# Kernel optimization log

Hardware: AMD Instinct MI355X
Metric: run time of the kernel (lower is better)

## Reference

```python
import jax, jax.numpy as jnp
import numpy as np
from functools import partial

N_TRAIN, N_FEAT, N_HID, ENC = 4096, 64, 256, 256
GH, AH, N_ANTES, MAX_LEN = 256, 64, 32768, 32


def setup_inputs() -> dict:
    key = jax.random.key(0)
    ks = jax.random.split(key, 14)
    sc = 0.05
    r = lambda k, shp: (jax.random.normal(k, shp, jnp.float32) * sc)
    return {
        'context': jax.random.normal(ks[0], (N_TRAIN, N_FEAT), jnp.float32),
        'S': jax.random.uniform(ks[1], (N_TRAIN, N_ANTES), jnp.float32),
        'enc_W1': r(ks[2], (N_FEAT, N_HID)), 'enc_b1': r(ks[3], (N_HID,)),
        'enc_W2': r(ks[4], (N_HID, ENC)), 'enc_b2': r(ks[5], (ENC,)),
        'W_ih': r(ks[6], (4 * GH, ENC)), 'W_hh': r(ks[7], (4 * GH, GH)),
        'b_ih': r(ks[8], (4 * GH,)), 'b_hh': r(ks[9], (4 * GH,)),
        'att_W1': r(ks[10], (N_TRAIN + GH, AH)), 'att_b1': r(ks[11], (AH,)),
        'att_w2': r(ks[12], (AH,)), 'att_b2': r(ks[13], (1,)),
        'max_len': MAX_LEN,
    }


def reference(context, S, enc_W1, enc_b1, enc_W2, enc_b2,
              W_ih, W_hh, b_ih, b_hh, att_W1, att_b1, att_w2, att_b2,
              max_len):
    n_train = context.shape[0]
    gh = W_hh.shape[1]
    # context encoder: Linear -> ReLU -> Linear  => phi [n_train, enc_dim]
    phi = jax.nn.relu(context @ enc_W1 + enc_b1) @ enc_W2 + enc_b2
    # LSTM input is phi at every step -> precompute input projection once
    x_proj = phi @ W_ih.T + b_ih + b_hh              # [n_train, 4*gh]
    # attention Linear over cat([S^T, e_t]) == S^T @ W1_S + e_t @ W1_h
    # S^T @ W1_S is step-invariant: precompute once  [n_antes, ah]
    S_proj = S.T @ att_W1[:n_train]
    W1_h = att_W1[n_train:]                          # [gh, ah]

    def step(carry, _):
        h, c = carry                                 # [n_train, gh] each
        gates = x_proj + h @ W_hh.T                  # [n_train, 4*gh]
        i, f, g, o = jnp.split(gates, 4, axis=-1)    # PyTorch gate order ifgo
        i, f, o = jax.nn.sigmoid(i), jax.nn.sigmoid(f), jax.nn.sigmoid(o)
        c = f * c + i * jnp.tanh(g)
        h = o * jnp.tanh(c)
        e_t = h.mean(axis=0)                         # mean over batch, [gh]
        hid = jax.nn.relu(S_proj + e_t @ W1_h + att_b1)   # [n_antes, ah]
        scores = hid @ att_w2 + att_b2[0]            # [n_antes]
        return (h, c), scores

    h0 = jnp.zeros((n_train, gh), x_proj.dtype)
    c0 = jnp.zeros((n_train, gh), x_proj.dtype)
    _, scores = jax.lax.scan(step, (h0, c0), None, length=max_len)
    idx = jnp.argmax(scores, axis=-1)                # d[t] = A[idx[t]]
    return scores, idx
```

## Files before the change

kernel.cpp:

```cpp
#include <hip/hip_runtime.h>
#include <hip/hip_bf16.h>
#include <math.h>

#define N_TRAIN 4096
#define N_FEAT  64
#define NHID    256
#define ENC     256
#define GH      256
#define AH      64
#define NANTES  32768
#define TSTEPS  32

#define SSTR 528

typedef __attribute__((ext_vector_type(8))) short bf16x8;
typedef __attribute__((ext_vector_type(4))) float f32x4;

#define BMFMA(a_, b_, c_) __builtin_amdgcn_mfma_f32_16x16x32_bf16(a_, b_, c_, 0, 0, 0)

__device__ __forceinline__ float sigmoidf_(float x) {
    return 1.0f / (1.0f + __expf(-x));
}
__device__ __forceinline__ float tanhf_(float x) {
    return 1.0f - 2.0f / (__expf(2.0f * x) + 1.0f);
}
__device__ __forceinline__ unsigned short f2bf_rne(float x) {
    unsigned int u = __float_as_uint(x);
    unsigned int r = u + 0x7FFFu + ((u >> 16) & 1u);
    return (unsigned short)(r >> 16);
}
__device__ __forceinline__ float bf2f(unsigned short b) {
    return __uint_as_float(((unsigned int)b) << 16);
}

__device__ __forceinline__ void async16(const void* g, void* l) {
    __builtin_amdgcn_global_load_lds(
        (const __attribute__((address_space(1))) void*)g,
        (__attribute__((address_space(3))) void*)l, 16, 0, 0);
}

__global__ void zero_kernel(float* __restrict__ esum) {
    int tid = blockIdx.x * blockDim.x + threadIdx.x;
    for (int i = tid; i < TSTEPS * GH; i += gridDim.x * blockDim.x)
        esum[i] = 0.0f;
}

__global__ void pack_whh(const float* __restrict__ Whh,
                         unsigned short* __restrict__ hi)
{
    int g = blockIdx.x * 256 + threadIdx.x;
    if (g >= 64 * 8 * 64) return;
    int lane  = g & 63;
    int ks    = (g >> 6) & 7;
    int ntile = g >> 9;
    int n  = ntile * 16 + (lane & 15);
    int k0 = ks * 32 + (lane >> 4) * 8;
    const float* src = Whh + n * 256 + k0;
    #pragma unroll
    for (int j = 0; j < 8; ++j)
        hi[g * 8 + j] = f2bf_rne(src[j]);
}

__global__ void pack_wa(const float* __restrict__ attW1,
                        unsigned short* __restrict__ hi,
                        unsigned short* __restrict__ lo)
{
    int g = blockIdx.x * 256 + threadIdx.x;
    if (g >= 4 * 128 * 64) return;
    int lane = g & 63;
    int ks   = (g >> 6) & 127;
    int ct   = g >> 13;
    int n  = ct * 16 + (lane & 15);
    int k0 = ks * 32 + (lane >> 4) * 8;
    const float* src = attW1 + (size_t)k0 * AH + n;
    #pragma unroll
    for (int j = 0; j < 8; ++j) {
        float x = src[(size_t)j * AH];
        unsigned short h16 = f2bf_rne(x);
        hi[g * 8 + j] = h16;
        lo[g * 8 + j] = f2bf_rne(x - bf2f(h16));
    }
}

__global__ __launch_bounds__(512, 2) void lstm_kernel(
    const float* __restrict__ ctx,
    const float* __restrict__ encW1, const float* __restrict__ encb1,
    const float* __restrict__ encW2, const float* __restrict__ encb2,
    const float* __restrict__ Wih,
    const float* __restrict__ bih,  const float* __restrict__ bhh,
    const unsigned short* __restrict__ Wph,
    float* __restrict__ esum)
{
    __shared__ char pool[98304];
    __shared__ short hhi[2][16 * 256];
    __shared__ short hlo[2][16 * 256];

    float* sbuf = (float*)pool;

    const int tid   = threadIdx.x;
    const int j     = tid & 255;
    const int rh    = tid >> 8;
    const int rbase = rh * 8;
    const int r0    = blockIdx.x * 16;

    {
        float acc[8];
        float b = encb1[j];
        #pragma unroll
        for (int r = 0; r < 8; ++r) acc[r] = b;
        for (int k = 0; k < N_FEAT; ++k) {
            float w = encW1[k * NHID + j];
            #pragma unroll
            for (int r = 0; r < 8; ++r)
                acc[r] = fmaf(ctx[(r0 + rbase + r) * N_FEAT + k], w, acc[r]);
        }
        #pragma unroll
        for (int r = 0; r < 8; ++r)
            sbuf[(rbase + r) * SSTR + j] = fmaxf(acc[r], 0.0f);
    }
    __syncthreads();

    {
        float p[8];
        float b = encb2[j];
        #pragma unroll
        for (int r = 0; r < 8; ++r) p[r] = b;
        for (int k = 0; k < NHID; ++k) {
            float w = encW2[k * ENC + j];
            #pragma unroll
            for (int r = 0; r < 8; ++r)
                p[r] = fmaf(sbuf[(rbase + r) * SSTR + k], w, p[r]);
        }
        __syncthreads();
        #pragma unroll
        for (int r = 0; r < 8; ++r)
            sbuf[(rbase + r) * SSTR + 264 + j] = p[r];
    }
    __syncthreads();

    float xp[4][8];
    #pragma unroll
    for (int g = 0; g < 4; ++g) {
        int m = g * 256 + j;
        float b = bih[m] + bhh[m];
        #pragma unroll
        for (int r = 0; r < 8; ++r) xp[g][r] = b;
        const float4* wrow = (const float4*)(Wih + m * ENC);
        for (int k4 = 0; k4 < ENC / 4; ++k4) {
            float4 wv = wrow[k4];
            #pragma unroll
            for (int r = 0; r < 8; ++r) {
                const float* ph = &sbuf[(rbase + r) * SSTR + 264 + k4 * 4];
                float v = xp[g][r];
                v = fmaf(ph[0], wv.x, v);
                v = fmaf(ph[1], wv.y, v);
                v = fmaf(ph[2], wv.z, v);
                v = fmaf(ph[3], wv.w, v);
                xp[g][r] = v;
            }
        }
    }
    __syncthreads();

    const int w    = tid >> 6;
    const int l    = tid & 63;
    const int col  = l & 15;
    const int kp   = l >> 4;
    const int arow = col;
    const int asw  = (arow & 7) << 3;

    f32x4 xpf[4][2];
    #pragma unroll 1
    for (int g = 0; g < 4; ++g) {
        #pragma unroll
        for (int r = 0; r < 8; ++r)
            sbuf[(rbase + r) * SSTR + j] = xp[g][r];
        __syncthreads();
        #pragma unroll
        for (int u = 0; u < 2; ++u)
            #pragma unroll
            for (int q = 0; q < 4; ++q)
                xpf[g][u][q] = sbuf[(kp * 4 + q) * SSTR + w * 32 + u * 16 + col];
        __syncthreads();
    }

    for (int i = tid; i < 16 * 256; i += 512) { hhi[0][i] = 0; hlo[0][i] = 0; }
    __syncthreads();

    const unsigned short* Bh = Wph + (size_t)l * 8;
    char* ra = pool + (w * 3 + 0) * 4096;
    char* rb = pool + (w * 3 + 1) * 4096;
    char* rc = pool + (w * 3 + 2) * 4096;
    const size_t lane16 = (size_t)l * 16;

#define ISSUE(base, gj) do {                                                 \
        const int u_ = (gj) >> 3, ks2_ = (gj) & 7;                           \
        _Pragma("unroll") for (int g_ = 0; g_ < 4; ++g_) {                   \
            const unsigned short* gp_ = Bh +                                 \
                (size_t)(((16 * g_ + 2 * w + u_) * 8 + ks2_) * 64) * 8;      \
            async16(gp_, (base) + g_ * 1024);                                \
        }                                                                    \
    } while (0)

#define CNS(base, gi) do {                                                   \
        asm volatile("s_waitcnt vmcnt(8)" ::: "memory");                     \
        __builtin_amdgcn_sched_barrier(0);                                   \
        const char* p_ = (base) + lane16;                                    \
        bf16x8 f0 = *(const bf16x8*)(p_);                                    \
        bf16x8 f1 = *(const bf16x8*)(p_ + 1024);                             \
        bf16x8 f2 = *(const bf16x8*)(p_ + 2048);                             \
        bf16x8 f3 = *(const bf16x8*)(p_ + 3072);                             \
        const int ks_ = (gi) & 7;                                            \
        bf16x8 ah = *(const bf16x8*)&Ahi[arow * 256 +                        \
                        ((ks_ * 32 + kp * 8) ^ asw)];                        \
        bf16x8 al = *(const bf16x8*)&Alo[arow * 256 +                        \
                        ((ks_ * 32 + kp * 8) ^ asw)];                        \
        acc[0] = BMFMA(al, f0, acc[0]); acc[0] = BMFMA(ah, f0, acc[0]);      \
        acc[1] = BMFMA(al, f1, acc[1]); acc[1] = BMFMA(ah, f1, acc[1]);      \
        acc[2] = BMFMA(al, f2, acc[2]); acc[2] = BMFMA(ah, f2, acc[2]);      \
        acc[3] = BMFMA(al, f3, acc[3]); acc[3] = BMFMA(ah, f3, acc[3]);      \
        asm volatile("" ::: "memory");                                       \
        ISSUE(base, ((gi) + 3) & 15);                                        \
    } while (0)

#define POINTW(u_) do {                                                      \
        float s = 0.0f;                                                      \
        _Pragma("unroll") for (int q = 0; q < 4; ++q) {                      \
            float iv = sigmoidf_(acc[0][q]);                                 \
            float fv = sigmoidf_(acc[1][q]);                                 \
            float gv = tanhf_   (acc[2][q]);                                 \
            float ov = sigmoidf_(acc[3][q]);                                 \
            c[u_][q] = fv * c[u_][q] + iv * gv;                              \
            float hv = ov * tanhf_(c[u_][q]);                                \
            s += hv;                                                         \
            unsigned short h16 = f2bf_rne(hv);                               \
            float lof = hv - bf2f(h16);                                      \
            int row  = kp * 4 + q;                                           \
            int hcol = w * 32 + (u_) * 16 + col;                             \
            int sidx = row * 256 + (hcol ^ ((row & 7) << 3));                \
            Nhi[sidx] = (short)h16;                                          \
            Nlo[sidx] = (short)f2bf_rne(lof);                                \
        }                                                                    \
        su[u_] = s;                                                          \
    } while (0)

    ISSUE(ra, 0); ISSUE(rb, 1); ISSUE(rc, 2);

    float c[2][4];
    #pragma unroll
    for (int u = 0; u < 2; ++u)
        #pragma unroll
        for (int q = 0; q < 4; ++q) c[u][q] = 0.0f;

    for (int t = 0; t < TSTEPS; ++t) {
        const short* Ahi = hhi[t & 1];
        const short* Alo = hlo[t & 1];
        short* Nhi = hhi[(t + 1) & 1];
        short* Nlo = hlo[(t + 1) & 1];

        float su[2];
        f32x4 acc[4];

        #pragma unroll
        for (int g = 0; g < 4; ++g) acc[g] = xpf[g][0];
        CNS(ra, 0); CNS(rb, 1); CNS(rc, 2); CNS(ra, 3);
        CNS(rb, 4); CNS(rc, 5); CNS(ra, 6); CNS(rb, 7);
        POINTW(0);

        #pragma unroll
        for (int g = 0; g < 4; ++g) acc[g] = xpf[g][1];
        CNS(rc, 8);  CNS(ra, 9);  CNS(rb, 10); CNS(rc, 11);
        CNS(ra, 12); CNS(rb, 13); CNS(rc, 14); CNS(ra, 15);
        POINTW(1);

        #pragma unroll
        for (int u = 0; u < 2; ++u) {
            float v = su[u];
            v += __shfl_xor(v, 16);
            v += __shfl_xor(v, 32);
            if (l < 16)
                atomicAdd(&esum[t * GH + w * 32 + u * 16 + l], v);
        }

        asm volatile("s_waitcnt lgkmcnt(0)" ::: "memory");
        __builtin_amdgcn_s_barrier();
        __builtin_amdgcn_sched_barrier(0);
        asm volatile("" ::: "memory");

        char* tp = ra; ra = rb; rb = rc; rc = tp;
    }
#undef ISSUE
#undef CNS
#undef POINTW
}

__global__ void proj_kernel(const float* __restrict__ esum,
                            const float* __restrict__ attW1,
                            const float* __restrict__ attb1,
                            float* __restrict__ proj)
{
    __shared__ float part[4][AH];
    const int t   = blockIdx.x;
    const int cix = threadIdx.x & 63;
    const int g   = threadIdx.x >> 6;
    float a = 0.0f;
    #pragma unroll 4
    for (int k = g * 64; k < g * 64 + 64; ++k) {
        float e = esum[t * GH + k] * (1.0f / (float)N_TRAIN);
        a = fmaf(e, attW1[(size_t)(N_TRAIN + k) * AH + cix], a);
    }
    part[g][cix] = a;
    __syncthreads();
    if (threadIdx.x < AH)
        proj[t * AH + cix] = part[0][cix] + part[1][cix] + part[2][cix] +
                             part[3][cix] + attb1[cix];
}

__global__ __launch_bounds__(512, 4) void scores_kernel(
    const float* __restrict__ S,
    const unsigned short* __restrict__ Wah,
    const unsigned short* __restrict__ Wal,
    const float* __restrict__ proj,
    const float* __restrict__ attw2,
    const float* __restrict__ attb2,
    float* __restrict__ out)
{
    __shared__ float projl[TSTEPS * AH];
    __shared__ float w2l[AH];

    const int tid   = threadIdx.x;
    const int wv    = tid >> 6;
    const int l     = tid & 63;
    const int kp    = l >> 4;
    const int atile = blockIdx.x * 128 + wv * 16;
    const int an    = atile + (l & 15);

    f32x4 acc[4];
    #pragma unroll
    for (int ct = 0; ct < 4; ++ct) acc[ct] = (f32x4){0.f, 0.f, 0.f, 0.f};

    const float* Sp = S + an;
    const unsigned short* Bh = Wah + (size_t)l * 8;
    const unsigned short* Bl = Wal + (size_t)l * 8;

#define LOADS(dst, ks_) do {                                                 \
        _Pragma("unroll") for (int jj = 0; jj < 8; ++jj)                     \
            dst[jj] = Sp[(size_t)(32 * (ks_) + kp * 8 + jj) * NANTES];       \
    } while (0)

    float sA[8], sB[8];
    LOADS(sA, 0);
    LOADS(sB, 1);

    #pragma unroll 2
    for (int ks = 0; ks < 128; ++ks) {
        bf16x8 bh[4], bl[4];
        #pragma unroll
        for (int ct = 0; ct < 4; ++ct) {
            size_t off = (size_t)((ct * 128 + ks) * 64) * 8;
            bh[ct] = *(const bf16x8*)(Bh + off);
            bl[ct] = *(const bf16x8*)(Bl + off);
        }

        float* cur = (ks & 1) ? sB : sA;
        bf16x8 ah, al;
        #pragma unroll
        for (int jj = 0; jj < 8; ++jj) {
            float x = cur[jj];
            unsigned short h16 = f2bf_rne(x);
            ah[jj] = (short)h16;
            al[jj] = (short)f2bf_rne(x - bf2f(h16));
        }

        if (ks < 126) LOADS(cur, ks + 2);

        #pragma unroll
        for (int ct = 0; ct < 4; ++ct) {
            acc[ct] = BMFMA(al, bl[ct], acc[ct]);
            acc[ct] = BMFMA(al, bh[ct], acc[ct]);
            acc[ct] = BMFMA(ah, bl[ct], acc[ct]);
            acc[ct] = BMFMA(ah, bh[ct], acc[ct]);
        }
    }
#undef LOADS

    for (int i = tid; i < TSTEPS * AH; i += 512) projl[i] = proj[i];
    if (tid < AH) w2l[tid] = attw2[tid];
    __syncthreads();

    const float b2v = attb2[0];
    const int cn = l & 15;
    #pragma unroll 1
    for (int t = 0; t < TSTEPS; ++t) {
        #pragma unroll
        for (int q = 0; q < 4; ++q) {
            float sc = 0.0f;
            #pragma unroll
            for (int ct = 0; ct < 4; ++ct) {
                int colg = ct * 16 + cn;
                sc += fmaxf(acc[ct][q] + projl[t * AH + colg], 0.0f) * w2l[colg];
            }
            sc += __shfl_xor(sc, 1);
            sc += __shfl_xor(sc, 2);
            sc += __shfl_xor(sc, 4);
            sc += __shfl_xor(sc, 8);
            if (cn == 0)
                out[(size_t)t * NANTES + atile + kp * 4 + q] = sc + b2v;
        }
    }
}

__global__ void argmax_kernel(const float* __restrict__ scores,
                              float* __restrict__ out)
{
    __shared__ float bv[256];
    __shared__ int   bidx[256];
    const int t = blockIdx.x, tid = threadIdx.x;
    float best = -INFINITY;
    int   bi   = 0x7fffffff;
    for (int a = tid; a < NANTES; a += 256) {
        float v = scores[(size_t)t * NANTES + a];
        if (v > best) { best = v; bi = a; }
    }
    bv[tid] = best; bidx[tid] = bi;
    __syncthreads();
    for (int s = 128; s > 0; s >>= 1) {
        if (tid < s) {
            if (bv[tid + s] > bv[tid] ||
                (bv[tid + s] == bv[tid] && bidx[tid + s] < bidx[tid])) {
                bv[tid] = bv[tid + s];
                bidx[tid] = bidx[tid + s];
            }
        }
        __syncthreads();
    }
    if (tid == 0)
        out[(size_t)TSTEPS * NANTES + t] = (float)bidx[0];
}

extern "C" void kernel_launch(void* const* d_in, const int* in_sizes, int n_in,
                              void* d_out, int out_size, void* d_ws, size_t ws_size,
                              hipStream_t stream)
{
    const float* ctx   = (const float*)d_in[0];
    const float* S     = (const float*)d_in[1];
    const float* encW1 = (const float*)d_in[2];
    const float* encb1 = (const float*)d_in[3];
    const float* encW2 = (const float*)d_in[4];
    const float* encb2 = (const float*)d_in[5];
    const float* Wih   = (const float*)d_in[6];
    const float* Whh   = (const float*)d_in[7];
    const float* bih   = (const float*)d_in[8];
    const float* bhh   = (const float*)d_in[9];
    const float* attW1 = (const float*)d_in[10];
    const float* attb1 = (const float*)d_in[11];
    const float* attw2 = (const float*)d_in[12];
    const float* attb2 = (const float*)d_in[13];

    char* ws = (char*)d_ws;
    float* esum = (float*)ws;
    float* proj = (float*)(ws + 32768);
    unsigned short* Wph = (unsigned short*)(ws + 40960);
    unsigned short* Wah = (unsigned short*)(ws + 40960 + 524288);
    unsigned short* Wal = (unsigned short*)(ws + 40960 + 1048576);
    float* out  = (float*)d_out;

    zero_kernel<<<dim3(8), dim3(256), 0, stream>>>(esum);
    pack_whh<<<dim3(128), dim3(256), 0, stream>>>(Whh, Wph);
    pack_wa<<<dim3(128), dim3(256), 0, stream>>>(attW1, Wah, Wal);
    lstm_kernel<<<dim3(N_TRAIN / 16), dim3(512), 0, stream>>>(
        ctx, encW1, encb1, encW2, encb2, Wih, bih, bhh, Wph, esum);
    proj_kernel<<<dim3(TSTEPS), dim3(256), 0, stream>>>(esum, attW1, attb1, proj);
    scores_kernel<<<dim3(NANTES / 128), dim3(512), 0, stream>>>(
        S, Wah, Wal, proj, attw2, attb2, out);
    argmax_kernel<<<dim3(TSTEPS), dim3(256), 0, stream>>>(out, out);
}
```

Before: 583.8 us.

## Double-buffer two k-slices per stage in LSTM recurrence and drop lo*lo MFMA term

The LSTM recurrent weight streaming changes from a three-buffer, one-k-slice-per-stage async pipeline to a two-buffer scheme in which each stage loads and consumes two k-slices. This halves the number of wait/issue points per timestep and lets more MFMAs run between waits. The per-stage buffers double, so the shared pool grows from 96 KB to 128 KB, which raises LDS pressure per block. A sched_barrier is also removed, giving the compiler more freedom to reorder. Separately, the scoring kernel drops the lo×lo bf16 MFMA term from its split-precision product, which slightly reduces accuracy in exchange for fewer MFMAs.

```diff
diff --git a/kernel.cpp b/kernel.cpp
--- a/kernel.cpp
+++ b/kernel.cpp
@@ -91,7 +91,7 @@
     const unsigned short* __restrict__ Wph,
     float* __restrict__ esum)
 {
-    __shared__ char pool[98304];
+    __shared__ char pool[131072];
     __shared__ short hhi[2][16 * 256];
     __shared__ short hlo[2][16 * 256];
 
@@ -187,40 +187,51 @@
     for (int i = tid; i < 16 * 256; i += 512) { hhi[0][i] = 0; hlo[0][i] = 0; }
     __syncthreads();
 
-    const unsigned short* Bh = Wph + (size_t)l * 8;
-    char* ra = pool + (w * 3 + 0) * 4096;
-    char* rb = pool + (w * 3 + 1) * 4096;
-    char* rc = pool + (w * 3 + 2) * 4096;
+    const unsigned short* Bw = Wph + (size_t)l * 8 + (size_t)w * 8192;
+    char* sA = pool + (w * 2 + 0) * 8192;
+    char* sB = pool + (w * 2 + 1) * 8192;
     const size_t lane16 = (size_t)l * 16;
 
-#define ISSUE(base, gj) do {                                                 \
-        const int u_ = (gj) >> 3, ks2_ = (gj) & 7;                           \
+#define ISSUE2(base, gj) do {                                                \
+        const int u_ = (gj) >> 3, ka_ = (gj) & 7, kb_ = ((gj) + 1) & 7;      \
         _Pragma("unroll") for (int g_ = 0; g_ < 4; ++g_) {                   \
-            const unsigned short* gp_ = Bh +                                 \
-                (size_t)(((16 * g_ + 2 * w + u_) * 8 + ks2_) * 64) * 8;      \
-            async16(gp_, (base) + g_ * 1024);                                \
+            async16(Bw + (size_t)(((16 * g_ + u_) * 8 + ka_) * 512),         \
+                    (base) + g_ * 1024);                                     \
+            async16(Bw + (size_t)(((16 * g_ + u_) * 8 + kb_) * 512),         \
+                    (base) + 4096 + g_ * 1024);                              \
         }                                                                    \
     } while (0)
 
-#define CNS(base, gi) do {                                                   \
+#define CNS2(base, gi) do {                                                  \
         asm volatile("s_waitcnt vmcnt(8)" ::: "memory");                     \
-        __builtin_amdgcn_sched_barrier(0);                                   \
         const char* p_ = (base) + lane16;                                    \
         bf16x8 f0 = *(const bf16x8*)(p_);                                    \
         bf16x8 f1 = *(const bf16x8*)(p_ + 1024);                             \
         bf16x8 f2 = *(const bf16x8*)(p_ + 2048);                             \
         bf16x8 f3 = *(const bf16x8*)(p_ + 3072);                             \
-        const int ks_ = (gi) & 7;                                            \
-        bf16x8 ah = *(const bf16x8*)&Ahi[arow * 256 +                        \
-                        ((ks_ * 32 + kp * 8) ^ asw)];                        \
-        bf16x8 al = *(const bf16x8*)&Alo[arow * 256 +                        \
-                        ((ks_ * 32 + kp * 8) ^ asw)];                        \
-        acc[0] = BMFMA(al, f0, acc[0]); acc[0] = BMFMA(ah, f0, acc[0]);      \
-        acc[1] = BMFMA(al, f1, acc[1]); acc[1] = BMFMA(ah, f1, acc[1]);      \
-        acc[2] = BMFMA(al, f2, acc[2]); acc[2] = BMFMA(ah, f2, acc[2]);      \
-        acc[3] = BMFMA(al, f3, acc[3]); acc[3] = BMFMA(ah, f3, acc[3]);      \
+        bf16x8 g0 = *(const bf16x8*)(p_ + 4096);                             \
+        bf16x8 g1 = *(const bf16x8*)(p_ + 5120);                             \
+        bf16x8 g2 = *(const bf16x8*)(p_ + 6144);                             \
+        bf16x8 g3 = *(const bf16x8*)(p_ + 7168);                             \
+        const int ka_ = (gi) & 7, kb_ = ((gi) + 1) & 7;                      \
+        bf16x8 ah0 = *(const bf16x8*)&Ahi[arow * 256 +                       \
+                         ((ka_ * 32 + kp * 8) ^ asw)];                       \
+        bf16x8 al0 = *(const bf16x8*)&Alo[arow * 256 +                       \
+                         ((ka_ * 32 + kp * 8) ^ asw)];                       \
+        bf16x8 ah1 = *(const bf16x8*)&Ahi[arow * 256 +                       \
+                         ((kb_ * 32 + kp * 8) ^ asw)];                       \
+        bf16x8 al1 = *(const bf16x8*)&Alo[arow * 256 +                       \
+                         ((kb_ * 32 + kp * 8) ^ asw)];                       \
+        acc[0] = BMFMA(al0, f0, acc[0]); acc[0] = BMFMA(ah0, f0, acc[0]);    \
+        acc[1] = BMFMA(al0, f1, acc[1]); acc[1] = BMFMA(ah0, f1, acc[1]);    \
+        acc[2] = BMFMA(al0, f2, acc[2]); acc[2] = BMFMA(ah0, f2, acc[2]);    \
+        acc[3] = BMFMA(al0, f3, acc[3]); acc[3] = BMFMA(ah0, f3, acc[3]);    \
+        acc[0] = BMFMA(al1, g0, acc[0]); acc[0] = BMFMA(ah1, g0, acc[0]);    \
+        acc[1] = BMFMA(al1, g1, acc[1]); acc[1] = BMFMA(ah1, g1, acc[1]);    \
+        acc[2] = BMFMA(al1, g2, acc[2]); acc[2] = BMFMA(ah1, g2, acc[2]);    \
+        acc[3] = BMFMA(al1, g3, acc[3]); acc[3] = BMFMA(ah1, g3, acc[3]);    \
         asm volatile("" ::: "memory");                                       \
-        ISSUE(base, ((gi) + 3) & 15);                                        \
+        ISSUE2(base, ((gi) + 4) & 15);                                       \
     } while (0)
 
 #define POINTW(u_) do {                                                      \
@@ -244,7 +255,7 @@
         su[u_] = s;                                                          \
     } while (0)
 
-    ISSUE(ra, 0); ISSUE(rb, 1); ISSUE(rc, 2);
+    ISSUE2(sA, 0); ISSUE2(sB, 2);
 
     float c[2][4];
     #pragma unroll
@@ -263,14 +274,12 @@
 
         #pragma unroll
         for (int g = 0; g < 4; ++g) acc[g] = xpf[g][0];
-        CNS(ra, 0); CNS(rb, 1); CNS(rc, 2); CNS(ra, 3);
-        CNS(rb, 4); CNS(rc, 5); CNS(ra, 6); CNS(rb, 7);
+        CNS2(sA, 0); CNS2(sB, 2); CNS2(sA, 4); CNS2(sB, 6);
         POINTW(0);
 
         #pragma unroll
         for (int g = 0; g < 4; ++g) acc[g] = xpf[g][1];
-        CNS(rc, 8);  CNS(ra, 9);  CNS(rb, 10); CNS(rc, 11);
-        CNS(ra, 12); CNS(rb, 13); CNS(rc, 14); CNS(ra, 15);
+        CNS2(sA, 8); CNS2(sB, 10); CNS2(sA, 12); CNS2(sB, 14);
         POINTW(1);
 
         #pragma unroll
@@ -286,11 +295,9 @@
         __builtin_amdgcn_s_barrier();
         __builtin_amdgcn_sched_barrier(0);
         asm volatile("" ::: "memory");
-
-        char* tp = ra; ra = rb; rb = rc; rc = tp;
-    }
-#undef ISSUE
-#undef CNS
+    }
+#undef ISSUE2
+#undef CNS2
 #undef POINTW
 }
 
@@ -376,7 +383,6 @@
 
         #pragma unroll
         for (int ct = 0; ct < 4; ++ct) {
-            acc[ct] = BMFMA(al, bl[ct], acc[ct]);
             acc[ct] = BMFMA(al, bh[ct], acc[ct]);
             acc[ct] = BMFMA(ah, bl[ct], acc[ct]);
             acc[ct] = BMFMA(ah, bh[ct], acc[ct]);
```

Result: slower. 598.9 us (+2.6%).

## Deepen LSTM weight prefetch ring to four stages and fuse prep kernels

Applied to the files above, without the earlier changes.

Replaces the three rotating 4KB LDS staging buffers per wave in the recurrent loop with a four-slot ring indexed by chunk number, issuing loads four chunks ahead with a relaxed vmcnt wait. This is meant to hide more global-load latency for the W_hh tiles. The LDS pool grows to 128KB, which pushes total LDS use near the per-CU limit. The zero and two packing kernels are merged into one launch to cut launch overhead, and the negligible lo*lo MFMA term in the scores split-precision GEMM is dropped.

```diff
diff --git a/kernel.cpp b/kernel.cpp
--- a/kernel.cpp
+++ b/kernel.cpp
@@ -39,46 +39,41 @@
         (__attribute__((address_space(3))) void*)l, 16, 0, 0);
 }
 
-__global__ void zero_kernel(float* __restrict__ esum) {
-    int tid = blockIdx.x * blockDim.x + threadIdx.x;
-    for (int i = tid; i < TSTEPS * GH; i += gridDim.x * blockDim.x)
-        esum[i] = 0.0f;
-}
-
-__global__ void pack_whh(const float* __restrict__ Whh,
-                         unsigned short* __restrict__ hi)
+__global__ void prep_kernel(const float* __restrict__ Whh,
+                            unsigned short* __restrict__ Wph,
+                            const float* __restrict__ attW1,
+                            unsigned short* __restrict__ Wah,
+                            unsigned short* __restrict__ Wal,
+                            float* __restrict__ esum)
 {
     int g = blockIdx.x * 256 + threadIdx.x;
-    if (g >= 64 * 8 * 64) return;
-    int lane  = g & 63;
-    int ks    = (g >> 6) & 7;
-    int ntile = g >> 9;
-    int n  = ntile * 16 + (lane & 15);
-    int k0 = ks * 32 + (lane >> 4) * 8;
-    const float* src = Whh + n * 256 + k0;
-    #pragma unroll
-    for (int j = 0; j < 8; ++j)
-        hi[g * 8 + j] = f2bf_rne(src[j]);
-}
-
-__global__ void pack_wa(const float* __restrict__ attW1,
-                        unsigned short* __restrict__ hi,
-                        unsigned short* __restrict__ lo)
-{
-    int g = blockIdx.x * 256 + threadIdx.x;
-    if (g >= 4 * 128 * 64) return;
-    int lane = g & 63;
-    int ks   = (g >> 6) & 127;
-    int ct   = g >> 13;
-    int n  = ct * 16 + (lane & 15);
-    int k0 = ks * 32 + (lane >> 4) * 8;
-    const float* src = attW1 + (size_t)k0 * AH + n;
-    #pragma unroll
-    for (int j = 0; j < 8; ++j) {
-        float x = src[(size_t)j * AH];
-        unsigned short h16 = f2bf_rne(x);
-        hi[g * 8 + j] = h16;
-        lo[g * 8 + j] = f2bf_rne(x - bf2f(h16));
+    if (g < TSTEPS * GH) esum[g] = 0.0f;
+
+    {
+        int lane  = g & 63;
+        int ks    = (g >> 6) & 7;
+        int ntile = g >> 9;
+        int n  = ntile * 16 + (lane & 15);
+        int k0 = ks * 32 + (lane >> 4) * 8;
+        const float* src = Whh + n * 256 + k0;
+        #pragma unroll
+        for (int jj = 0; jj < 8; ++jj)
+            Wph[g * 8 + jj] = f2bf_rne(src[jj]);
+    }
+    {
+        int lane = g & 63;
+        int ks   = (g >> 6) & 127;
+        int ct   = g >> 13;
+        int n  = ct * 16 + (lane & 15);
+        int k0 = ks * 32 + (lane >> 4) * 8;
+        const float* src = attW1 + (size_t)k0 * AH + n;
+        #pragma unroll
+        for (int jj = 0; jj < 8; ++jj) {
+            float x = src[(size_t)jj * AH];
+            unsigned short h16 = f2bf_rne(x);
+            Wah[g * 8 + jj] = h16;
+            Wal[g * 8 + jj] = f2bf_rne(x - bf2f(h16));
+        }
     }
 }
 
@@ -91,7 +86,7 @@
     const unsigned short* __restrict__ Wph,
     float* __restrict__ esum)
 {
-    __shared__ char pool[98304];
+    __shared__ char pool[131072];
     __shared__ short hhi[2][16 * 256];
     __shared__ short hlo[2][16 * 256];
 
@@ -187,25 +182,22 @@
     for (int i = tid; i < 16 * 256; i += 512) { hhi[0][i] = 0; hlo[0][i] = 0; }
     __syncthreads();
 
-    const unsigned short* Bh = Wph + (size_t)l * 8;
-    char* ra = pool + (w * 3 + 0) * 4096;
-    char* rb = pool + (w * 3 + 1) * 4096;
-    char* rc = pool + (w * 3 + 2) * 4096;
+    const unsigned short* Bw = Wph + (size_t)l * 8 + (size_t)w * 8192;
+    char* ringw = pool + w * 16384;
     const size_t lane16 = (size_t)l * 16;
 
-#define ISSUE(base, gj) do {                                                 \
-        const int u_ = (gj) >> 3, ks2_ = (gj) & 7;                           \
-        _Pragma("unroll") for (int g_ = 0; g_ < 4; ++g_) {                   \
-            const unsigned short* gp_ = Bh +                                 \
-                (size_t)(((16 * g_ + 2 * w + u_) * 8 + ks2_) * 64) * 8;      \
-            async16(gp_, (base) + g_ * 1024);                                \
-        }                                                                    \
+#define ISSUE(gj) do {                                                       \
+        const int gm_ = (gj) & 15;                                           \
+        const int u_ = gm_ >> 3, ks_ = gm_ & 7;                              \
+        char* base_ = ringw + (gm_ & 3) * 4096;                              \
+        _Pragma("unroll") for (int g_ = 0; g_ < 4; ++g_)                     \
+            async16(Bw + (size_t)(((16 * g_ + u_) * 8 + ks_) * 512),         \
+                    base_ + g_ * 1024);                                      \
     } while (0)
 
-#define CNS(base, gi) do {                                                   \
-        asm volatile("s_waitcnt vmcnt(8)" ::: "memory");                     \
-        __builtin_amdgcn_sched_barrier(0);                                   \
-        const char* p_ = (base) + lane16;                                    \
+#define CNS(gi) do {                                                         \
+        asm volatile("s_waitcnt vmcnt(12)" ::: "memory");                    \
+        const char* p_ = ringw + ((gi) & 3) * 4096 + lane16;                 \
         bf16x8 f0 = *(const bf16x8*)(p_);                                    \
         bf16x8 f1 = *(const bf16x8*)(p_ + 1024);                             \
         bf16x8 f2 = *(const bf16x8*)(p_ + 2048);                             \
@@ -220,7 +212,7 @@
         acc[2] = BMFMA(al, f2, acc[2]); acc[2] = BMFMA(ah, f2, acc[2]);      \
         acc[3] = BMFMA(al, f3, acc[3]); acc[3] = BMFMA(ah, f3, acc[3]);      \
         asm volatile("" ::: "memory");                                       \
-        ISSUE(base, ((gi) + 3) & 15);                                        \
+        ISSUE((gi) + 4);                                                     \
     } while (0)
 
 #define POINTW(u_) do {                                                      \
@@ -244,7 +236,7 @@
         su[u_] = s;                                                          \
     } while (0)
 
-    ISSUE(ra, 0); ISSUE(rb, 1); ISSUE(rc, 2);
+    ISSUE(0); ISSUE(1); ISSUE(2); ISSUE(3);
 
     float c[2][4];
     #pragma unroll
@@ -263,14 +255,14 @@
 
         #pragma unroll
         for (int g = 0; g < 4; ++g) acc[g] = xpf[g][0];
-        CNS(ra, 0); CNS(rb, 1); CNS(rc, 2); CNS(ra, 3);
-        CNS(rb, 4); CNS(rc, 5); CNS(ra, 6); CNS(rb, 7);
+        CNS(0); CNS(1); CNS(2); CNS(3);
+        CNS(4); CNS(5); CNS(6); CNS(7);
         POINTW(0);
 
         #pragma unroll
         for (int g = 0; g < 4; ++g) acc[g] = xpf[g][1];
-        CNS(rc, 8);  CNS(ra, 9);  CNS(rb, 10); CNS(rc, 11);
-        CNS(ra, 12); CNS(rb, 13); CNS(rc, 14); CNS(ra, 15);
+        CNS(8);  CNS(9);  CNS(10); CNS(11);
+        CNS(12); CNS(13); CNS(14); CNS(15);
         POINTW(1);
 
         #pragma unroll
@@ -286,8 +278,6 @@
         __builtin_amdgcn_s_barrier();
         __builtin_amdgcn_sched_barrier(0);
         asm volatile("" ::: "memory");
-
-        char* tp = ra; ra = rb; rb = rc; rc = tp;
     }
 #undef ISSUE
 #undef CNS
@@ -376,7 +366,6 @@
 
         #pragma unroll
         for (int ct = 0; ct < 4; ++ct) {
-            acc[ct] = BMFMA(al, bl[ct], acc[ct]);
             acc[ct] = BMFMA(al, bh[ct], acc[ct]);
             acc[ct] = BMFMA(ah, bl[ct], acc[ct]);
             acc[ct] = BMFMA(ah, bh[ct], acc[ct]);
@@ -465,9 +454,7 @@
     unsigned short* Wal = (unsigned short*)(ws + 40960 + 1048576);
     float* out  = (float*)d_out;
 
-    zero_kernel<<<dim3(8), dim3(256), 0, stream>>>(esum);
-    pack_whh<<<dim3(128), dim3(256), 0, stream>>>(Whh, Wph);
-    pack_wa<<<dim3(128), dim3(256), 0, stream>>>(attW1, Wah, Wal);
+    prep_kernel<<<dim3(128), dim3(256), 0, stream>>>(Whh, Wph, attW1, Wah, Wal, esum);
     lstm_kernel<<<dim3(N_TRAIN / 16), dim3(512), 0, stream>>>(
         ctx, encW1, encb1, encW2, encb2, Wih, bih, bhh, Wph, esum);
     proj_kernel<<<dim3(TSTEPS), dim3(256), 0, stream>>>(esum, attW1, attb1, proj);
```

Result: no change. 586.1 us (+0.4%).

## Compute LSTM input projection with bf16 MFMA and merge prep kernels

Applied to the files above, without the earlier changes.

The per-thread fp32 FMA loop for the x_proj input projection (phi @ W_ih^T) is replaced by bf16 MFMA using a prepacked W_ih. phi is split into hi and lo bf16 parts in LDS and feeds the MFMA accumulators directly, which also drops the LDS round trip that reshuffled xp into fragment layout. The three preparation kernels are merged into one launch that also packs W_ih. The scores kernel drops the lo*lo MFMA term. Precision falls slightly because W_ih is stored only as bf16 hi and the lo*lo product is gone, which could change argmax ties.

```diff
diff --git a/kernel.cpp b/kernel.cpp
--- a/kernel.cpp
+++ b/kernel.cpp
@@ -39,46 +39,46 @@
         (__attribute__((address_space(3))) void*)l, 16, 0, 0);
 }
 
-__global__ void zero_kernel(float* __restrict__ esum) {
-    int tid = blockIdx.x * blockDim.x + threadIdx.x;
-    for (int i = tid; i < TSTEPS * GH; i += gridDim.x * blockDim.x)
-        esum[i] = 0.0f;
-}
-
-__global__ void pack_whh(const float* __restrict__ Whh,
-                         unsigned short* __restrict__ hi)
+__global__ void prep_kernel(const float* __restrict__ Whh,
+                            unsigned short* __restrict__ Wph,
+                            const float* __restrict__ Wih,
+                            unsigned short* __restrict__ Wpi,
+                            const float* __restrict__ attW1,
+                            unsigned short* __restrict__ Wah,
+                            unsigned short* __restrict__ Wal,
+                            float* __restrict__ esum)
 {
     int g = blockIdx.x * 256 + threadIdx.x;
-    if (g >= 64 * 8 * 64) return;
-    int lane  = g & 63;
-    int ks    = (g >> 6) & 7;
-    int ntile = g >> 9;
-    int n  = ntile * 16 + (lane & 15);
-    int k0 = ks * 32 + (lane >> 4) * 8;
-    const float* src = Whh + n * 256 + k0;
-    #pragma unroll
-    for (int j = 0; j < 8; ++j)
-        hi[g * 8 + j] = f2bf_rne(src[j]);
-}
-
-__global__ void pack_wa(const float* __restrict__ attW1,
-                        unsigned short* __restrict__ hi,
-                        unsigned short* __restrict__ lo)
-{
-    int g = blockIdx.x * 256 + threadIdx.x;
-    if (g >= 4 * 128 * 64) return;
-    int lane = g & 63;
-    int ks   = (g >> 6) & 127;
-    int ct   = g >> 13;
-    int n  = ct * 16 + (lane & 15);
-    int k0 = ks * 32 + (lane >> 4) * 8;
-    const float* src = attW1 + (size_t)k0 * AH + n;
-    #pragma unroll
-    for (int j = 0; j < 8; ++j) {
-        float x = src[(size_t)j * AH];
-        unsigned short h16 = f2bf_rne(x);
-        hi[g * 8 + j] = h16;
-        lo[g * 8 + j] = f2bf_rne(x - bf2f(h16));
+    if (g < TSTEPS * GH) esum[g] = 0.0f;
+
+    {
+        int lane  = g & 63;
+        int ks    = (g >> 6) & 7;
+        int ntile = g >> 9;
+        int n  = ntile * 16 + (lane & 15);
+        int k0 = ks * 32 + (lane >> 4) * 8;
+        const float* src1 = Whh + n * 256 + k0;
+        const float* src2 = Wih + n * 256 + k0;
+        #pragma unroll
+        for (int jj = 0; jj < 8; ++jj) {
+            Wph[g * 8 + jj] = f2bf_rne(src1[jj]);
+            Wpi[g * 8 + jj] = f2bf_rne(src2[jj]);
+        }
+    }
+    {
+        int lane = g & 63;
+        int ks   = (g >> 6) & 127;
+        int ct   = g >> 13;
+        int n  = ct * 16 + (lane & 15);
+        int k0 = ks * 32 + (lane >> 4) * 8;
+        const float* src = attW1 + (size_t)k0 * AH + n;
+        #pragma unroll
+        for (int jj = 0; jj < 8; ++jj) {
+            float x = src[(size_t)jj * AH];
+            unsigned short h16 = f2bf_rne(x);
+            Wah[g * 8 + jj] = h16;
+            Wal[g * 8 + jj] = f2bf_rne(x - bf2f(h16));
+        }
     }
 }
 
@@ -86,9 +86,9 @@
     const float* __restrict__ ctx,
     const float* __restrict__ encW1, const float* __restrict__ encb1,
     const float* __restrict__ encW2, const float* __restrict__ encb2,
-    const float* __restrict__ Wih,
     const float* __restrict__ bih,  const float* __restrict__ bhh,
     const unsigned short* __restrict__ Wph,
+    const unsigned short* __restrict__ Wpi,
     float* __restrict__ esum)
 {
     __shared__ char pool[98304];
@@ -102,65 +102,6 @@
     const int rh    = tid >> 8;
     const int rbase = rh * 8;
     const int r0    = blockIdx.x * 16;
-
-    {
-        float acc[8];
-        float b = encb1[j];
-        #pragma unroll
-        for (int r = 0; r < 8; ++r) acc[r] = b;
-        for (int k = 0; k < N_FEAT; ++k) {
-            float w = encW1[k * NHID + j];
-            #pragma unroll
-            for (int r = 0; r < 8; ++r)
-                acc[r] = fmaf(ctx[(r0 + rbase + r) * N_FEAT + k], w, acc[r]);
-        }
-        #pragma unroll
-        for (int r = 0; r < 8; ++r)
-            sbuf[(rbase + r) * SSTR + j] = fmaxf(acc[r], 0.0f);
-    }
-    __syncthreads();
-
-    {
-        float p[8];
-        float b = encb2[j];
-        #pragma unroll
-        for (int r = 0; r < 8; ++r) p[r] = b;
-        for (int k = 0; k < NHID; ++k) {
-            float w = encW2[k * ENC + j];
-            #pragma unroll
-            for (int r = 0; r < 8; ++r)
-                p[r] = fmaf(sbuf[(rbase + r) * SSTR + k], w, p[r]);
-        }
-        __syncthreads();
-        #pragma unroll
-        for (int r = 0; r < 8; ++r)
-            sbuf[(rbase + r) * SSTR + 264 + j] = p[r];
-    }
-    __syncthreads();
-
-    float xp[4][8];
-    #pragma unroll
-    for (int g = 0; g < 4; ++g) {
-        int m = g * 256 + j;
-        float b = bih[m] + bhh[m];
-        #pragma unroll
-        for (int r = 0; r < 8; ++r) xp[g][r] = b;
-        const float4* wrow = (const float4*)(Wih + m * ENC);
-        for (int k4 = 0; k4 < ENC / 4; ++k4) {
-            float4 wv = wrow[k4];
-            #pragma unroll
-            for (int r = 0; r < 8; ++r) {
-                const float* ph = &sbuf[(rbase + r) * SSTR + 264 + k4 * 4];
-                float v = xp[g][r];
-                v = fmaf(ph[0], wv.x, v);
-                v = fmaf(ph[1], wv.y, v);
-                v = fmaf(ph[2], wv.z, v);
-                v = fmaf(ph[3], wv.w, v);
-                xp[g][r] = v;
-            }
-        }
-    }
-    __syncthreads();
 
     const int w    = tid >> 6;
     const int l    = tid & 63;
@@ -169,22 +110,110 @@
     const int arow = col;
     const int asw  = (arow & 7) << 3;
 
+    {
+        float acc[8];
+        float b = encb1[j];
+        #pragma unroll
+        for (int r = 0; r < 8; ++r) acc[r] = b;
+        for (int k = 0; k < N_FEAT; ++k) {
+            float wv = encW1[k * NHID + j];
+            #pragma unroll
+            for (int r = 0; r < 8; ++r)
+                acc[r] = fmaf(ctx[(r0 + rbase + r) * N_FEAT + k], wv, acc[r]);
+        }
+        #pragma unroll
+        for (int r = 0; r < 8; ++r)
+            sbuf[(rbase + r) * SSTR + j] = fmaxf(acc[r], 0.0f);
+    }
+    __syncthreads();
+
+    {
+        float p[8];
+        float b = encb2[j];
+        #pragma unroll
+        for (int r = 0; r < 8; ++r) p[r] = b;
+        for (int k4 = 0; k4 < NHID / 4; ++k4) {
+            float w0 = encW2[(k4 * 4 + 0) * ENC + j];
+            float w1 = encW2[(k4 * 4 + 1) * ENC + j];
+            float w2 = encW2[(k4 * 4 + 2) * ENC + j];
+            float w3 = encW2[(k4 * 4 + 3) * ENC + j];
+            #pragma unroll
+            for (int r = 0; r < 8; ++r) {
+                const f32x4 hv = *(const f32x4*)&sbuf[(rbase + r) * SSTR + k4 * 4];
+                float v = p[r];
+                v = fmaf(hv[0], w0, v);
+                v = fmaf(hv[1], w1, v);
+                v = fmaf(hv[2], w2, v);
+                v = fmaf(hv[3], w3, v);
+                p[r] = v;
+            }
+        }
+        #pragma unroll
+        for (int r = 0; r < 8; ++r) {
+            int row = rbase + r;
+            unsigned short h16 = f2bf_rne(p[r]);
+            float lof = p[r] - bf2f(h16);
+            int sidx = row * 256 + (j ^ ((row & 7) << 3));
+            hhi[1][sidx] = (short)h16;
+            hlo[1][sidx] = (short)f2bf_rne(lof);
+        }
+    }
+    for (int i = tid; i < 16 * 256; i += 512) { hhi[0][i] = 0; hlo[0][i] = 0; }
+    __syncthreads();
+
     f32x4 xpf[4][2];
-    #pragma unroll 1
-    for (int g = 0; g < 4; ++g) {
-        #pragma unroll
-        for (int r = 0; r < 8; ++r)
-            sbuf[(rbase + r) * SSTR + j] = xp[g][r];
-        __syncthreads();
-        #pragma unroll
-        for (int u = 0; u < 2; ++u)
-            #pragma unroll
-            for (int q = 0; q < 4; ++q)
-                xpf[g][u][q] = sbuf[(kp * 4 + q) * SSTR + w * 32 + u * 16 + col];
-        __syncthreads();
-    }
-
-    for (int i = tid; i < 16 * 256; i += 512) { hhi[0][i] = 0; hlo[0][i] = 0; }
+    #pragma unroll
+    for (int g = 0; g < 4; ++g)
+        #pragma unroll
+        for (int u = 0; u < 2; ++u) {
+            int m = g * 256 + w * 32 + u * 16 + col;
+            float b = bih[m] + bhh[m];
+            xpf[g][u] = (f32x4){b, b, b, b};
+        }
+
+    const unsigned short* Wi2 = Wpi + (size_t)l * 8 + (size_t)w * 8192;
+
+#define XLOAD(dst, gj) do {                                                  \
+        const int u_ = (gj) >> 3, ks_ = (gj) & 7;                            \
+        _Pragma("unroll") for (int g_ = 0; g_ < 4; ++g_)                     \
+            dst[g_] = *(const bf16x8*)(Wi2 +                                 \
+                (size_t)(((16 * g_ + u_) * 8 + ks_) * 512));                 \
+    } while (0)
+
+#define XMFG(b_, gj, u_) do {                                                \
+        const int ks_ = (gj) & 7;                                            \
+        bf16x8 ah = *(const bf16x8*)&hhi[1][arow * 256 +                     \
+                        ((ks_ * 32 + kp * 8) ^ asw)];                        \
+        bf16x8 al = *(const bf16x8*)&hlo[1][arow * 256 +                     \
+                        ((ks_ * 32 + kp * 8) ^ asw)];                        \
+        _Pragma("unroll") for (int g_ = 0; g_ < 4; ++g_) {                   \
+            xpf[g_][u_] = BMFMA(al, b_[g_], xpf[g_][u_]);                    \
+            xpf[g_][u_] = BMFMA(ah, b_[g_], xpf[g_][u_]);                    \
+        }                                                                    \
+    } while (0)
+
+    {
+        bf16x8 xA[4], xB[4];
+        XLOAD(xA, 0); XLOAD(xB, 1);
+        XMFG(xA, 0, 0);  XLOAD(xA, 2);
+        XMFG(xB, 1, 0);  XLOAD(xB, 3);
+        XMFG(xA, 2, 0);  XLOAD(xA, 4);
+        XMFG(xB, 3, 0);  XLOAD(xB, 5);
+        XMFG(xA, 4, 0);  XLOAD(xA, 6);
+        XMFG(xB, 5, 0);  XLOAD(xB, 7);
+        XMFG(xA, 6, 0);  XLOAD(xA, 8);
+        XMFG(xB, 7, 0);  XLOAD(xB, 9);
+        XMFG(xA, 8, 1);  XLOAD(xA, 10);
+        XMFG(xB, 9, 1);  XLOAD(xB, 11);
+        XMFG(xA, 10, 1); XLOAD(xA, 12);
+        XMFG(xB, 11, 1); XLOAD(xB, 13);
+        XMFG(xA, 12, 1); XLOAD(xA, 14);
+        XMFG(xB, 13, 1); XLOAD(xB, 15);
+        XMFG(xA, 14, 1);
+        XMFG(xB, 15, 1);
+    }
+#undef XLOAD
+#undef XMFG
     __syncthreads();
 
     const unsigned short* Bh = Wph + (size_t)l * 8;
@@ -376,7 +405,6 @@
 
         #pragma unroll
         for (int ct = 0; ct < 4; ++ct) {
-            acc[ct] = BMFMA(al, bl[ct], acc[ct]);
             acc[ct] = BMFMA(al, bh[ct], acc[ct]);
             acc[ct] = BMFMA(ah, bl[ct], acc[ct]);
             acc[ct] = BMFMA(ah, bh[ct], acc[ct]);
@@ -463,13 +491,13 @@
     unsigned short* Wph = (unsigned short*)(ws + 40960);
     unsigned short* Wah = (unsigned short*)(ws + 40960 + 524288);
     unsigned short* Wal = (unsigned short*)(ws + 40960 + 1048576);
+    unsigned short* Wpi = (unsigned short*)(ws + 40960 + 1572864);
     float* out  = (float*)d_out;
 
-    zero_kernel<<<dim3(8), dim3(256), 0, stream>>>(esum);
-    pack_whh<<<dim3(128), dim3(256), 0, stream>>>(Whh, Wph);
-    pack_wa<<<dim3(128), dim3(256), 0, stream>>>(attW1, Wah, Wal);
+    prep_kernel<<<dim3(128), dim3(256), 0, stream>>>(
+        Whh, Wph, Wih, Wpi, attW1, Wah, Wal, esum);
     lstm_kernel<<<dim3(N_TRAIN / 16), dim3(512), 0, stream>>>(
-        ctx, encW1, encb1, encW2, encb2, Wih, bih, bhh, Wph, esum);
+        ctx, encW1, encb1, encW2, encb2, bih, bhh, Wph, Wpi, esum);
     proj_kernel<<<dim3(TSTEPS), dim3(256), 0, stream>>>(esum, attW1, attb1, proj);
     scores_kernel<<<dim3(NANTES / 128), dim3(512), 0, stream>>>(
         S, Wah, Wal, proj, attw2, attb2, out);
```

Measured after the change: 506.2 us, median of 2. 13.3% less time.
